# Optimization experiments

Hardware: AMD Instinct MI355X
Metric: run time of the kernel (lower is better)

The kernel has to match this reference:

```python
import jax, jax.numpy as jnp
import numpy as np

NEG_SLOPE = 0.2  # DGL GATConv default negative_slope


def gat_conv(x, W, attn_l, attn_r, bias, src, dst, n_nodes):
    """DGL-style GATConv. x:[N,F_in], W:[F_in,H*D], attn_l/attn_r/bias:[H,D].
    Returns [N,H,D]."""
    H, D = attn_l.shape
    feat = (x @ W).reshape(n_nodes, H, D)            # projected features
    el = jnp.sum(feat * attn_l, axis=-1)              # [N,H]
    er = jnp.sum(feat * attn_r, axis=-1)              # [N,H]
    e = jax.nn.leaky_relu(el[src] + er[dst], NEG_SLOPE)  # [E,H] per-edge score
    # edge softmax over incoming edges of each dst node (numerically stable)
    m = jax.ops.segment_max(e, dst, num_segments=n_nodes)   # [N,H]
    a = jnp.exp(e - m[dst])
    denom = jax.ops.segment_sum(a, dst, num_segments=n_nodes)
    alpha = a / denom[dst]                            # [E,H]
    msg = feat[src] * alpha[..., None]                # [E,H,D]
    out = jax.ops.segment_sum(msg, dst, num_segments=n_nodes)  # [N,H,D]
    return out + bias


def setup_inputs() -> dict:
    key = jax.random.key(0)
    ks = jax.random.split(key, 12)
    N, E = 50000, 800000
    F_in, D1, H1, F_out = 128, 32, 4, 64
    h = jax.random.normal(ks[0], (N, F_in), dtype=jnp.float32)
    src = jax.random.randint(ks[1], (E,), 0, N, dtype=jnp.int32)
    dst = jax.random.randint(ks[2], (E,), 0, N, dtype=jnp.int32)
    s1 = 1.0 / np.sqrt(F_in)
    s2 = 1.0 / np.sqrt(H1 * D1)
    W1 = jax.random.normal(ks[3], (F_in, H1 * D1), dtype=jnp.float32) * s1
    al1 = jax.random.normal(ks[4], (H1, D1), dtype=jnp.float32) * s1
    ar1 = jax.random.normal(ks[5], (H1, D1), dtype=jnp.float32) * s1
    b1 = jnp.zeros((H1, D1), dtype=jnp.float32)
    W2 = jax.random.normal(ks[6], (H1 * D1, 1 * F_out), dtype=jnp.float32) * s2
    al2 = jax.random.normal(ks[7], (1, F_out), dtype=jnp.float32) * s2
    ar2 = jax.random.normal(ks[8], (1, F_out), dtype=jnp.float32) * s2
    b2 = jnp.zeros((1, F_out), dtype=jnp.float32)
    return {"h": h, "src": src, "dst": dst,
            "W1": W1, "al1": al1, "ar1": ar1, "b1": b1,
            "W2": W2, "al2": al2, "ar2": ar2, "b2": b2}


def reference(h, src, dst, W1, al1, ar1, b1, W2, al2, ar2, b2):
    N = h.shape[0]
    x = gat_conv(h, W1, al1, ar1, b1, src, dst, N)   # [N,H,D]
    x = jax.nn.relu(x.reshape(N, -1))                # flatten heads + ReLU
    # dropout(p=0.2) is identity in eval mode
    x = gat_conv(x, W2, al2, ar2, b2, src, dst, N)   # [N,1,F_out]
    return x.squeeze(1)
```

## Files before the change

### kernel.cpp

```cpp
#include <hip/hip_runtime.h>

#define NEG_SLOPE 0.2f
#define CH 4096
#define DCAP 2048

__device__ inline unsigned short f2bf(float f) {
    unsigned u = __float_as_uint(f);
    unsigned r = (u + 0x7FFFu + ((u >> 16) & 1u)) >> 16;
    return (unsigned short)r;
}
__device__ inline unsigned pack2bf(float a, float b) {
    return (unsigned)f2bf(a) | ((unsigned)f2bf(b) << 16);
}
__device__ inline float bf2f(unsigned short s) {
    return __uint_as_float(((unsigned)s) << 16);
}
__device__ inline float bf2f_lo(unsigned u) { return __uint_as_float(u << 16); }
__device__ inline float bf2f_hi(unsigned u) { return __uint_as_float(u & 0xFFFF0000u); }
__device__ inline void wave_lds_fence() {
    asm volatile("s_waitcnt lgkmcnt(0)" ::: "memory");
}

__global__ __launch_bounds__(256) void bucketAB_kernel(const int* __restrict__ dst,
                                                       int* __restrict__ bucket_cnt,
                                                       int* __restrict__ bucket_base,
                                                       int* __restrict__ bucket_cursor,
                                                       int* __restrict__ row_start,
                                                       int N, int NB, int E) {
    __shared__ int lh[1024];
    __shared__ int psum[256];
    __shared__ int ticket_sh;
    const int tid = threadIdx.x;
    for (int i = tid; i < 1024; i += 256) lh[i] = 0;
    __syncthreads();
    const int base = blockIdx.x * CH;
    const int cnt = min(CH, E - base);
    for (int i = tid; i < cnt; i += 256) atomicAdd(&lh[dst[base + i] >> 6], 1);
    __syncthreads();
    for (int b = tid; b < NB; b += 256)
        if (lh[b]) atomicAdd(&bucket_cnt[b], lh[b]);
    __syncthreads();
    if (tid == 0) {
        __threadfence();
        ticket_sh = atomicAdd(&bucket_cnt[NB], 1);
    }
    __syncthreads();
    if (ticket_sh != (int)gridDim.x - 1) return;
    for (int i = tid; i < 1024; i += 256)
        lh[i] = (i < NB) ? atomicAdd(&bucket_cnt[i], 0) : 0;
    __syncthreads();
    int s0 = lh[tid * 4], s1 = lh[tid * 4 + 1], s2 = lh[tid * 4 + 2], s3 = lh[tid * 4 + 3];
    int tot = s0 + s1 + s2 + s3;
    psum[tid] = tot;
    __syncthreads();
    for (int off = 1; off < 256; off <<= 1) {
        int t = (tid >= off) ? psum[tid - off] : 0;
        __syncthreads();
        psum[tid] += t;
        __syncthreads();
    }
    int ebase = psum[tid] - tot;
    int e0 = ebase, e1 = ebase + s0, e2 = ebase + s0 + s1, e3 = ebase + s0 + s1 + s2;
    int i0 = tid * 4;
    if (i0 < NB)     { bucket_base[i0]     = e0; bucket_cursor[i0]     = e0; }
    if (i0 + 1 < NB) { bucket_base[i0 + 1] = e1; bucket_cursor[i0 + 1] = e1; }
    if (i0 + 2 < NB) { bucket_base[i0 + 2] = e2; bucket_cursor[i0 + 2] = e2; }
    if (i0 + 3 < NB) { bucket_base[i0 + 3] = e3; bucket_cursor[i0 + 3] = e3; }
    if (tid == 255) bucket_base[NB] = psum[255];
    if (tid == 0) row_start[N] = E;
}

__global__ __launch_bounds__(256) void csrC_gemm1_kernel(
    const int* __restrict__ src, const int* __restrict__ dst,
    int* __restrict__ bucket_cursor, unsigned* __restrict__ tmp, int E, int NB,
    int nchunks, const float* __restrict__ h, const float* __restrict__ W1,
    const float* __restrict__ al1, const float* __restrict__ ar1,
    unsigned short* __restrict__ feat1b, float* __restrict__ el1,
    float* __restrict__ er1, int N) {
    __shared__ __align__(16) int smem[8448];
    const int tid = threadIdx.x;
    if ((int)blockIdx.x < nchunks) {
        int* lh = smem;
        int* lex = smem + 1024;
        int* lcur = smem + 2048;
        int* gbase_sh = smem + 3072;
        int* psum = smem + 4096;
        unsigned* sortedv = (unsigned*)(smem + 4352);
        const int base_e = blockIdx.x * CH;
        const int cnt_e = min(CH, E - base_e);
        for (int i = tid; i < 1024; i += 256) lh[i] = 0;
        __syncthreads();
        for (int i = tid; i < cnt_e; i += 256) atomicAdd(&lh[dst[base_e + i] >> 6], 1);
        __syncthreads();
        int s0 = lh[tid * 4], s1 = lh[tid * 4 + 1], s2 = lh[tid * 4 + 2], s3 = lh[tid * 4 + 3];
        int tot = s0 + s1 + s2 + s3;
        psum[tid] = tot;
        __syncthreads();
        for (int off = 1; off < 256; off <<= 1) {
            int t = (tid >= off) ? psum[tid - off] : 0;
            __syncthreads();
            psum[tid] += t;
            __syncthreads();
        }
        int ebase = psum[tid] - tot;
        lex[tid * 4] = ebase;
        lex[tid * 4 + 1] = ebase + s0;
        lex[tid * 4 + 2] = ebase + s0 + s1;
        lex[tid * 4 + 3] = ebase + s0 + s1 + s2;
        __syncthreads();
        for (int b = tid; b < NB; b += 256) {
            int c = lh[b];
            gbase_sh[b] = c ? atomicAdd(&bucket_cursor[b], c) : 0;
            lcur[b] = 0;
        }
        __syncthreads();
        for (int i = tid; i < cnt_e; i += 256) {
            int e = base_e + i;
            int d = dst[e];
            unsigned b = (unsigned)d >> 6;
            int r = atomicAdd(&lcur[b], 1);
            sortedv[lex[b] + r] =
                (b << 22) | ((unsigned)(d & 63) << 16) | (unsigned)(src[e] & 0xFFFF);
        }
        __syncthreads();
        for (int i = tid; i < cnt_e; i += 256) {
            unsigned v = sortedv[i];
            int b = v >> 22;
            tmp[gbase_sh[b] + (i - lex[b])] = v;
        }
    } else {
        float* xs = (float*)smem;
        const int row0 = ((int)blockIdx.x - nchunks) * 64;
        {
            const float4* s4 = (const float4*)h;
            float4* d4 = (float4*)xs;
            int base4 = row0 * 32;
            int tot4 = N * 32;
            for (int i = tid; i < 2048; i += 256)
                if (base4 + i < tot4) d4[i] = s4[base4 + i];
        }
        __syncthreads();
        const int lane = tid & 31;
        const int c0 = lane * 4;
        const int r0 = (tid >> 5) * 8;
        float acc[8][4] = {};
#pragma unroll 4
        for (int k = 0; k < 128; ++k) {
            float4 w = *(const float4*)(W1 + k * 128 + c0);
#pragma unroll
            for (int r = 0; r < 8; ++r) {
                float x = xs[(r0 + r) * 128 + k];
                acc[r][0] = fmaf(x, w.x, acc[r][0]);
                acc[r][1] = fmaf(x, w.y, acc[r][1]);
                acc[r][2] = fmaf(x, w.z, acc[r][2]);
                acc[r][3] = fmaf(x, w.w, acc[r][3]);
            }
        }
        float4 alv = *(const float4*)(al1 + c0);
        float4 arv = *(const float4*)(ar1 + c0);
#pragma unroll
        for (int r = 0; r < 8; ++r) {
            int row = row0 + r0 + r;
            if (row < N) {
                ushort4 fb;
                fb.x = f2bf(acc[r][0]);
                fb.y = f2bf(acc[r][1]);
                fb.z = f2bf(acc[r][2]);
                fb.w = f2bf(acc[r][3]);
                *(ushort4*)(feat1b + (size_t)row * 128 + c0) = fb;
                float pl = acc[r][0] * alv.x + acc[r][1] * alv.y + acc[r][2] * alv.z +
                           acc[r][3] * alv.w;
                float pr = acc[r][0] * arv.x + acc[r][1] * arv.y + acc[r][2] * arv.z +
                           acc[r][3] * arv.w;
#pragma unroll
                for (int off = 4; off >= 1; off >>= 1) {
                    pl += __shfl_xor(pl, off, 32);
                    pr += __shfl_xor(pr, off, 32);
                }
                if ((lane & 7) == 0) {
                    el1[row * 4 + (lane >> 3)] = pl;
                    er1[row * 4 + (lane >> 3)] = pr;
                }
            }
        }
    }
}

__global__ __launch_bounds__(256) void bucketD_kernel(const unsigned* __restrict__ tmp,
                                                      const int* __restrict__ bucket_base,
                                                      int* __restrict__ srcs,
                                                      int* __restrict__ row_start,
                                                      int N, int NB) {
    __shared__ unsigned sval[DCAP];
    __shared__ int ssrc[DCAP];
    __shared__ int dh[64], dex[64], dcur[64];
    const int b = blockIdx.x;
    const int tid = threadIdx.x;
    const int gb = bucket_base[b], ge = bucket_base[b + 1];
    const int cnt = ge - gb;
    if (tid < 64) dh[tid] = 0;
    __syncthreads();
    if (cnt <= DCAP) {
        for (int i = tid; i < cnt; i += 256) {
            unsigned v = tmp[gb + i];
            sval[i] = v;
            atomicAdd(&dh[(v >> 16) & 63], 1);
        }
        __syncthreads();
        if (tid < 64) {
            int v = dh[tid], inc = v;
            for (int off = 1; off < 64; off <<= 1) {
                int t = __shfl_up(inc, off, 64);
                if (tid >= off) inc += t;
            }
            dex[tid] = inc - v;
            dcur[tid] = 0;
            int dglob = b * 64 + tid;
            if (dglob < N) row_start[dglob] = gb + inc - v;
        }
        __syncthreads();
        for (int i = tid; i < cnt; i += 256) {
            unsigned val = sval[i];
            int dl = (val >> 16) & 63;
            int r = atomicAdd(&dcur[dl], 1);
            ssrc[dex[dl] + r] = (int)(val & 0xFFFFu);
        }
        __syncthreads();
        for (int i = tid; i < cnt; i += 256) srcs[gb + i] = ssrc[i];
    } else {
        for (int i = tid; i < cnt; i += 256) atomicAdd(&dh[(tmp[gb + i] >> 16) & 63], 1);
        __syncthreads();
        if (tid < 64) {
            int v = dh[tid], inc = v;
            for (int off = 1; off < 64; off <<= 1) {
                int t = __shfl_up(inc, off, 64);
                if (tid >= off) inc += t;
            }
            dex[tid] = inc - v;
            dcur[tid] = 0;
            int dglob = b * 64 + tid;
            if (dglob < N) row_start[dglob] = gb + inc - v;
        }
        __syncthreads();
        for (int i = tid; i < cnt; i += 256) {
            unsigned val = tmp[gb + i];
            int dl = (val >> 16) & 63;
            int r = atomicAdd(&dcur[dl], 1);
            srcs[gb + dex[dl] + r] = (int)(val & 0xFFFFu);
        }
    }
}

__global__ __launch_bounds__(256) void gemm2_fused(const unsigned short* __restrict__ out1b,
                                                   const float* __restrict__ W2,
                                                   const float* __restrict__ al2,
                                                   const float* __restrict__ ar2,
                                                   unsigned short* __restrict__ feat2b,
                                                   float* __restrict__ el2,
                                                   float* __restrict__ er2, int N) {
    __shared__ float xs[64 * 128];
    const int tid = threadIdx.x;
    const int row0 = blockIdx.x * 64;
    {
        const uint4* s8 = (const uint4*)out1b;
        int base8 = row0 * 16;
        int tot8 = N * 16;
        for (int i = tid; i < 1024; i += 256)
            if (base8 + i < tot8) {
                uint4 v = s8[base8 + i];
                float* o = xs + i * 8;
                o[0] = bf2f_lo(v.x);
                o[1] = bf2f_hi(v.x);
                o[2] = bf2f_lo(v.y);
                o[3] = bf2f_hi(v.y);
                o[4] = bf2f_lo(v.z);
                o[5] = bf2f_hi(v.z);
                o[6] = bf2f_lo(v.w);
                o[7] = bf2f_hi(v.w);
            }
    }
    __syncthreads();
    const int lane = tid & 15;
    const int c0 = lane * 4;
    const int r0 = (tid >> 4) * 4;
    float acc[4][4] = {};
#pragma unroll 4
    for (int k = 0; k < 128; ++k) {
        float4 w = *(const float4*)(W2 + k * 64 + c0);
#pragma unroll
        for (int r = 0; r < 4; ++r) {
            float x = xs[(r0 + r) * 128 + k];
            acc[r][0] = fmaf(x, w.x, acc[r][0]);
            acc[r][1] = fmaf(x, w.y, acc[r][1]);
            acc[r][2] = fmaf(x, w.z, acc[r][2]);
            acc[r][3] = fmaf(x, w.w, acc[r][3]);
        }
    }
    float4 alv = *(const float4*)(al2 + c0);
    float4 arv = *(const float4*)(ar2 + c0);
#pragma unroll
    for (int r = 0; r < 4; ++r) {
        int row = row0 + r0 + r;
        if (row < N) {
            ushort4 fb;
            fb.x = f2bf(acc[r][0]);
            fb.y = f2bf(acc[r][1]);
            fb.z = f2bf(acc[r][2]);
            fb.w = f2bf(acc[r][3]);
            *(ushort4*)(feat2b + (size_t)row * 64 + c0) = fb;
            float pl = acc[r][0] * alv.x + acc[r][1] * alv.y + acc[r][2] * alv.z +
                       acc[r][3] * alv.w;
            float pr = acc[r][0] * arv.x + acc[r][1] * arv.y + acc[r][2] * arv.z +
                       acc[r][3] * arv.w;
#pragma unroll
            for (int off = 8; off >= 1; off >>= 1) {
                pl += __shfl_xor(pl, off, 16);
                pr += __shfl_xor(pr, off, 16);
            }
            if (lane == 0) {
                el2[row] = pl;
                er2[row] = pr;
            }
        }
    }
}

__global__ __launch_bounds__(256) void gather1_kernel(const int* __restrict__ row_start,
                                                      const int* __restrict__ srcs,
                                                      const float* __restrict__ el1,
                                                      const float* __restrict__ er1,
                                                      const unsigned short* __restrict__ feat1b,
                                                      const float* __restrict__ b1,
                                                      unsigned short* __restrict__ out1b,
                                                      int N) {
    __shared__ int s_sh[4][64];
    __shared__ float a_sh[4][256];
    const int tid = threadIdx.x;
    const int w = tid >> 6;
    const int lane = tid & 63;
    const int d = blockIdx.x * 4 + w;
    if (d >= N) return;
    const int beg = row_start[d], end = row_start[d + 1];
    const int q = lane >> 4;
    const int l16 = lane & 15;
    const int c0 = l16 * 8;
    const int h = l16 >> 2;
    float4 er4 = *(const float4*)(er1 + (size_t)d * 4);
    float acc[8] = {}, bcc[8] = {};
    float den = 0.f;
    for (int k0 = beg; k0 < end; k0 += 64) {
        const int M = min(64, end - k0);
        if (lane < M) {
            int s = srcs[k0 + lane];
            s_sh[w][lane] = s;
            float4 el4 = *(const float4*)(el1 + (size_t)s * 4);
            float v0 = el4.x + er4.x;
            float v1 = el4.y + er4.y;
            float v2 = el4.z + er4.z;
            float v3 = el4.w + er4.w;
            v0 = v0 > 0.f ? v0 : NEG_SLOPE * v0;
            v1 = v1 > 0.f ? v1 : NEG_SLOPE * v1;
            v2 = v2 > 0.f ? v2 : NEG_SLOPE * v2;
            v3 = v3 > 0.f ? v3 : NEG_SLOPE * v3;
            a_sh[w][lane * 4 + 0] = __expf(v0);
            a_sh[w][lane * 4 + 1] = __expf(v1);
            a_sh[w][lane * 4 + 2] = __expf(v2);
            a_sh[w][lane * 4 + 3] = __expf(v3);
        }
        wave_lds_fence();
        int e = q;
        for (; e + 4 < M; e += 8) {
            int s0 = s_sh[w][e], s1 = s_sh[w][e + 4];
            float a0 = a_sh[w][e * 4 + h];
            float a1 = a_sh[w][(e + 4) * 4 + h];
            uint4 f0 = *(const uint4*)(feat1b + (size_t)s0 * 128 + c0);
            uint4 f1 = *(const uint4*)(feat1b + (size_t)s1 * 128 + c0);
            den += a0 + a1;
            acc[0] = fmaf(bf2f_lo(f0.x), a0, acc[0]);
            acc[1] = fmaf(bf2f_hi(f0.x), a0, acc[1]);
            acc[2] = fmaf(bf2f_lo(f0.y), a0, acc[2]);
            acc[3] = fmaf(bf2f_hi(f0.y), a0, acc[3]);
            acc[4] = fmaf(bf2f_lo(f0.z), a0, acc[4]);
            acc[5] = fmaf(bf2f_hi(f0.z), a0, acc[5]);
            acc[6] = fmaf(bf2f_lo(f0.w), a0, acc[6]);
            acc[7] = fmaf(bf2f_hi(f0.w), a0, acc[7]);
            bcc[0] = fmaf(bf2f_lo(f1.x), a1, bcc[0]);
            bcc[1] = fmaf(bf2f_hi(f1.x), a1, bcc[1]);
            bcc[2] = fmaf(bf2f_lo(f1.y), a1, bcc[2]);
            bcc[3] = fmaf(bf2f_hi(f1.y), a1, bcc[3]);
            bcc[4] = fmaf(bf2f_lo(f1.z), a1, bcc[4]);
            bcc[5] = fmaf(bf2f_hi(f1.z), a1, bcc[5]);
            bcc[6] = fmaf(bf2f_lo(f1.w), a1, bcc[6]);
            bcc[7] = fmaf(bf2f_hi(f1.w), a1, bcc[7]);
        }
        while (e < M) {
            int s0 = s_sh[w][e];
            float a0 = a_sh[w][e * 4 + h];
            uint4 f0 = *(const uint4*)(feat1b + (size_t)s0 * 128 + c0);
            den += a0;
            acc[0] = fmaf(bf2f_lo(f0.x), a0, acc[0]);
            acc[1] = fmaf(bf2f_hi(f0.x), a0, acc[1]);
            acc[2] = fmaf(bf2f_lo(f0.y), a0, acc[2]);
            acc[3] = fmaf(bf2f_hi(f0.y), a0, acc[3]);
            acc[4] = fmaf(bf2f_lo(f0.z), a0, acc[4]);
            acc[5] = fmaf(bf2f_hi(f0.z), a0, acc[5]);
            acc[6] = fmaf(bf2f_lo(f0.w), a0, acc[6]);
            acc[7] = fmaf(bf2f_hi(f0.w), a0, acc[7]);
            e += 4;
        }
        wave_lds_fence();
    }
#pragma unroll
    for (int j = 0; j < 8; ++j) {
        acc[j] += bcc[j];
        acc[j] += __shfl_xor(acc[j], 16, 64);
        acc[j] += __shfl_xor(acc[j], 32, 64);
    }
    den += __shfl_xor(den, 16, 64);
    den += __shfl_xor(den, 32, 64);
    if (q == 0) {
        float inv = (end > beg) ? 1.f / den : 0.f;
        float4 bv0 = *(const float4*)(b1 + c0);
        float4 bv1 = *(const float4*)(b1 + c0 + 4);
        uint4 o;
        o.x = pack2bf(fmaxf(acc[0] * inv + bv0.x, 0.f), fmaxf(acc[1] * inv + bv0.y, 0.f));
        o.y = pack2bf(fmaxf(acc[2] * inv + bv0.z, 0.f), fmaxf(acc[3] * inv + bv0.w, 0.f));
        o.z = pack2bf(fmaxf(acc[4] * inv + bv1.x, 0.f), fmaxf(acc[5] * inv + bv1.y, 0.f));
        o.w = pack2bf(fmaxf(acc[6] * inv + bv1.z, 0.f), fmaxf(acc[7] * inv + bv1.w, 0.f));
        *(uint4*)(out1b + (size_t)d * 128 + c0) = o;
    }
}

__global__ __launch_bounds__(256) void gather2_kernel(const int* __restrict__ row_start,
                                                      const int* __restrict__ srcs,
                                                      const float* __restrict__ el2,
                                                      const float* __restrict__ er2,
                                                      const unsigned short* __restrict__ feat2b,
                                                      const float* __restrict__ b2,
                                                      float* __restrict__ out2, int N) {
    __shared__ int s_sh[4][64];
    __shared__ float a_sh[4][64];
    const int tid = threadIdx.x;
    const int w = tid >> 6;
    const int lane = tid & 63;
    const int d = blockIdx.x * 4 + w;
    if (d >= N) return;
    const int beg = row_start[d], end = row_start[d + 1];
    const int q = lane >> 4;
    const int l16 = lane & 15;
    const int c0 = l16 * 4;
    const float er_d = er2[d];
    float acc[4] = {}, bcc[4] = {};
    float den = 0.f;
    for (int k0 = beg; k0 < end; k0 += 64) {
        const int M = min(64, end - k0);
        if (lane < M) {
            int s = srcs[k0 + lane];
            s_sh[w][lane] = s;
            float v = el2[s] + er_d;
            v = v > 0.f ? v : NEG_SLOPE * v;
            a_sh[w][lane] = __expf(v);
        }
        wave_lds_fence();
        int e = q;
        for (; e + 4 < M; e += 8) {
            int s0 = s_sh[w][e], s1 = s_sh[w][e + 4];
            float a0 = a_sh[w][e], a1 = a_sh[w][e + 4];
            uint2 f0 = *(const uint2*)(feat2b + (size_t)s0 * 64 + c0);
            uint2 f1 = *(const uint2*)(feat2b + (size_t)s1 * 64 + c0);
            den += a0 + a1;
            acc[0] = fmaf(bf2f_lo(f0.x), a0, acc[0]);
            acc[1] = fmaf(bf2f_hi(f0.x), a0, acc[1]);
            acc[2] = fmaf(bf2f_lo(f0.y), a0, acc[2]);
            acc[3] = fmaf(bf2f_hi(f0.y), a0, acc[3]);
            bcc[0] = fmaf(bf2f_lo(f1.x), a1, bcc[0]);
            bcc[1] = fmaf(bf2f_hi(f1.x), a1, bcc[1]);
            bcc[2] = fmaf(bf2f_lo(f1.y), a1, bcc[2]);
            bcc[3] = fmaf(bf2f_hi(f1.y), a1, bcc[3]);
        }
        while (e < M) {
            int s0 = s_sh[w][e];
            float a0 = a_sh[w][e];
            uint2 f0 = *(const uint2*)(feat2b + (size_t)s0 * 64 + c0);
            den += a0;
            acc[0] = fmaf(bf2f_lo(f0.x), a0, acc[0]);
            acc[1] = fmaf(bf2f_hi(f0.x), a0, acc[1]);
            acc[2] = fmaf(bf2f_lo(f0.y), a0, acc[2]);
            acc[3] = fmaf(bf2f_hi(f0.y), a0, acc[3]);
            e += 4;
        }
        wave_lds_fence();
    }
#pragma unroll
    for (int j = 0; j < 4; ++j) {
        acc[j] += bcc[j];
        acc[j] += __shfl_xor(acc[j], 16, 64);
        acc[j] += __shfl_xor(acc[j], 32, 64);
    }
    den += __shfl_xor(den, 16, 64);
    den += __shfl_xor(den, 32, 64);
    if (q == 0) {
        float inv = (end > beg) ? 1.f / den : 0.f;
        float4 bv = *(const float4*)(b2 + c0);
        *(float4*)(out2 + (size_t)d * 64 + c0) =
            make_float4(acc[0] * inv + bv.x, acc[1] * inv + bv.y, acc[2] * inv + bv.z,
                        acc[3] * inv + bv.w);
    }
}

extern "C" void kernel_launch(void* const* d_in, const int* in_sizes, int n_in,
                              void* d_out, int out_size, void* d_ws, size_t ws_size,
                              hipStream_t stream) {
    const float* h   = (const float*)d_in[0];
    const int*   src = (const int*)d_in[1];
    const int*   dst = (const int*)d_in[2];
    const float* W1  = (const float*)d_in[3];
    const float* al1 = (const float*)d_in[4];
    const float* ar1 = (const float*)d_in[5];
    const float* b1  = (const float*)d_in[6];
    const float* W2  = (const float*)d_in[7];
    const float* al2 = (const float*)d_in[8];
    const float* ar2 = (const float*)d_in[9];
    const float* b2  = (const float*)d_in[10];

    const int N = in_sizes[0] / 128;
    const int E = in_sizes[1];
    const int NB = (N + 63) >> 6;

    char* ws = (char*)d_ws;
    size_t off = 0;
    auto alloc = [&](size_t elems) -> void* {
        void* p = (void*)(ws + off);
        off += ((elems * 4 + 255) / 256) * 256;
        return p;
    };
    int* bucket_cnt    = (int*)alloc(NB + 1);
    int* bucket_base   = (int*)alloc(NB + 1);
    int* bucket_cursor = (int*)alloc(NB);
    unsigned* tmp      = (unsigned*)alloc(E);
    int* srcs          = (int*)alloc(E);
    int* row_start     = (int*)alloc(N + 1);
    float* el1   = (float*)alloc((size_t)N * 4);
    float* er1   = (float*)alloc((size_t)N * 4);
    unsigned short* feat1b = (unsigned short*)alloc((size_t)N * 64);
    unsigned short* out1b  = (unsigned short*)alloc((size_t)N * 64);
    float* el2   = (float*)alloc(N);
    float* er2   = (float*)alloc(N);
    unsigned short* feat2b = (unsigned short*)alloc((size_t)N * 32);
    float* out2  = (float*)d_out;

    const int nchunks = (E + CH - 1) / CH;
    const int gemm1_blocks = (N + 63) / 64;

    hipMemsetAsync(bucket_cnt, 0, (size_t)(NB + 1) * 4, stream);
    bucketAB_kernel<<<nchunks, 256, 0, stream>>>(dst, bucket_cnt, bucket_base,
                                                 bucket_cursor, row_start, N, NB, E);
    csrC_gemm1_kernel<<<nchunks + gemm1_blocks, 256, 0, stream>>>(
        src, dst, bucket_cursor, tmp, E, NB, nchunks, h, W1, al1, ar1, feat1b, el1,
        er1, N);
    bucketD_kernel<<<NB, 256, 0, stream>>>(tmp, bucket_base, srcs, row_start, N, NB);

    gather1_kernel<<<(N + 3) / 4, 256, 0, stream>>>(row_start, srcs, el1, er1, feat1b,
                                                    b1, out1b, N);

    gemm2_fused<<<(N + 63) / 64, 256, 0, stream>>>(out1b, W2, al2, ar2, feat2b, el2,
                                                   er2, N);
    gather2_kernel<<<(N + 3) / 4, 256, 0, stream>>>(row_start, srcs, el2, er2, feat2b,
                                                    b2, out2, N);
}
```

Before: 221.2 us.

## Fuse bucket histogram into CSR scatter kernel with grid-wide spin barrier; widen gather2 loads

The separate bucket counting/prefix kernel is merged into the CSR-scatter+GEMM1 kernel. Each chunk block publishes its histogram, the last block to arrive computes the bucket prefix sums and sets a ready flag, and all chunk blocks spin on that flag before claiming scatter offsets. This removes one kernel launch and one re-read of dst, but it depends on every chunk block being co-resident, which risks deadlock if they are not. Separately, gather2 now has each lane load 8 bf16 features (uint4) instead of 4, with one extra shuffle stage, so fewer, wider loads are issued per edge.

```diff
diff --git a/kernel.cpp b/kernel.cpp
--- a/kernel.cpp
+++ b/kernel.cpp
@@ -21,59 +21,12 @@
     asm volatile("s_waitcnt lgkmcnt(0)" ::: "memory");
 }
 
-__global__ __launch_bounds__(256) void bucketAB_kernel(const int* __restrict__ dst,
-                                                       int* __restrict__ bucket_cnt,
-                                                       int* __restrict__ bucket_base,
-                                                       int* __restrict__ bucket_cursor,
-                                                       int* __restrict__ row_start,
-                                                       int N, int NB, int E) {
-    __shared__ int lh[1024];
-    __shared__ int psum[256];
-    __shared__ int ticket_sh;
-    const int tid = threadIdx.x;
-    for (int i = tid; i < 1024; i += 256) lh[i] = 0;
-    __syncthreads();
-    const int base = blockIdx.x * CH;
-    const int cnt = min(CH, E - base);
-    for (int i = tid; i < cnt; i += 256) atomicAdd(&lh[dst[base + i] >> 6], 1);
-    __syncthreads();
-    for (int b = tid; b < NB; b += 256)
-        if (lh[b]) atomicAdd(&bucket_cnt[b], lh[b]);
-    __syncthreads();
-    if (tid == 0) {
-        __threadfence();
-        ticket_sh = atomicAdd(&bucket_cnt[NB], 1);
-    }
-    __syncthreads();
-    if (ticket_sh != (int)gridDim.x - 1) return;
-    for (int i = tid; i < 1024; i += 256)
-        lh[i] = (i < NB) ? atomicAdd(&bucket_cnt[i], 0) : 0;
-    __syncthreads();
-    int s0 = lh[tid * 4], s1 = lh[tid * 4 + 1], s2 = lh[tid * 4 + 2], s3 = lh[tid * 4 + 3];
-    int tot = s0 + s1 + s2 + s3;
-    psum[tid] = tot;
-    __syncthreads();
-    for (int off = 1; off < 256; off <<= 1) {
-        int t = (tid >= off) ? psum[tid - off] : 0;
-        __syncthreads();
-        psum[tid] += t;
-        __syncthreads();
-    }
-    int ebase = psum[tid] - tot;
-    int e0 = ebase, e1 = ebase + s0, e2 = ebase + s0 + s1, e3 = ebase + s0 + s1 + s2;
-    int i0 = tid * 4;
-    if (i0 < NB)     { bucket_base[i0]     = e0; bucket_cursor[i0]     = e0; }
-    if (i0 + 1 < NB) { bucket_base[i0 + 1] = e1; bucket_cursor[i0 + 1] = e1; }
-    if (i0 + 2 < NB) { bucket_base[i0 + 2] = e2; bucket_cursor[i0 + 2] = e2; }
-    if (i0 + 3 < NB) { bucket_base[i0 + 3] = e3; bucket_cursor[i0 + 3] = e3; }
-    if (tid == 255) bucket_base[NB] = psum[255];
-    if (tid == 0) row_start[N] = E;
-}
-
-__global__ __launch_bounds__(256) void csrC_gemm1_kernel(
+__global__ __launch_bounds__(256) void csrABC_gemm1_kernel(
     const int* __restrict__ src, const int* __restrict__ dst,
-    int* __restrict__ bucket_cursor, unsigned* __restrict__ tmp, int E, int NB,
-    int nchunks, const float* __restrict__ h, const float* __restrict__ W1,
+    int* __restrict__ bucket_cnt, int* __restrict__ bucket_base,
+    int* __restrict__ bucket_cursor, int* __restrict__ row_start,
+    unsigned* __restrict__ tmp, int E, int NB, int nchunks,
+    const float* __restrict__ h, const float* __restrict__ W1,
     const float* __restrict__ al1, const float* __restrict__ ar1,
     unsigned short* __restrict__ feat1b, float* __restrict__ el1,
     float* __restrict__ er1, int N) {
@@ -92,6 +45,45 @@
         __syncthreads();
         for (int i = tid; i < cnt_e; i += 256) atomicAdd(&lh[dst[base_e + i] >> 6], 1);
         __syncthreads();
+        for (int b = tid; b < NB; b += 256)
+            if (lh[b]) atomicAdd(&bucket_cnt[b], lh[b]);
+        __syncthreads();
+        __shared__ int ticket_sh;
+        if (tid == 0) {
+            __threadfence();
+            ticket_sh = atomicAdd(&bucket_cnt[NB], 1);
+        }
+        __syncthreads();
+        if (ticket_sh == nchunks - 1) {
+            for (int i = tid; i < 1024; i += 256)
+                lcur[i] = (i < NB) ? atomicAdd(&bucket_cnt[i], 0) : 0;
+            __syncthreads();
+            int c0s = lcur[tid * 4], c1s = lcur[tid * 4 + 1], c2s = lcur[tid * 4 + 2],
+                c3s = lcur[tid * 4 + 3];
+            int tot = c0s + c1s + c2s + c3s;
+            psum[tid] = tot;
+            __syncthreads();
+            for (int off = 1; off < 256; off <<= 1) {
+                int t = (tid >= off) ? psum[tid - off] : 0;
+                __syncthreads();
+                psum[tid] += t;
+                __syncthreads();
+            }
+            int eb = psum[tid] - tot;
+            int i0 = tid * 4;
+            if (i0 < NB)     { bucket_base[i0]     = eb;               atomicExch(&bucket_cursor[i0], eb); }
+            if (i0 + 1 < NB) { bucket_base[i0 + 1] = eb + c0s;         atomicExch(&bucket_cursor[i0 + 1], eb + c0s); }
+            if (i0 + 2 < NB) { bucket_base[i0 + 2] = eb + c0s + c1s;   atomicExch(&bucket_cursor[i0 + 2], eb + c0s + c1s); }
+            if (i0 + 3 < NB) { bucket_base[i0 + 3] = eb + c0s + c1s + c2s;
+                               atomicExch(&bucket_cursor[i0 + 3], eb + c0s + c1s + c2s); }
+            if (tid == 255) bucket_base[NB] = psum[255];
+            if (tid == 0) row_start[N] = E;
+            __syncthreads();
+            if (tid == 0) {
+                __threadfence();
+                atomicExch(&bucket_cnt[NB + 1], 1);
+            }
+        }
         int s0 = lh[tid * 4], s1 = lh[tid * 4 + 1], s2 = lh[tid * 4 + 2], s3 = lh[tid * 4 + 3];
         int tot = s0 + s1 + s2 + s3;
         psum[tid] = tot;
@@ -108,17 +100,24 @@
         lex[tid * 4 + 2] = ebase + s0 + s1;
         lex[tid * 4 + 3] = ebase + s0 + s1 + s2;
         __syncthreads();
+        __shared__ int ready_sh;
+        if (tid == 0) {
+            while (atomicAdd(&bucket_cnt[NB + 1], 0) == 0) {}
+            ready_sh = 1;
+        }
+        __syncthreads();
+        (void)ready_sh;
         for (int b = tid; b < NB; b += 256) {
             int c = lh[b];
             gbase_sh[b] = c ? atomicAdd(&bucket_cursor[b], c) : 0;
-            lcur[b] = 0;
+            lh[b] = 0;
         }
         __syncthreads();
         for (int i = tid; i < cnt_e; i += 256) {
             int e = base_e + i;
             int d = dst[e];
             unsigned b = (unsigned)d >> 6;
-            int r = atomicAdd(&lcur[b], 1);
+            int r = atomicAdd(&lh[b], 1);
             sortedv[lex[b] + r] =
                 (b << 22) | ((unsigned)(d & 63) << 16) | (unsigned)(src[e] & 0xFFFF);
         }
@@ -446,11 +445,11 @@
     const int d = blockIdx.x * 4 + w;
     if (d >= N) return;
     const int beg = row_start[d], end = row_start[d + 1];
-    const int q = lane >> 4;
-    const int l16 = lane & 15;
-    const int c0 = l16 * 4;
+    const int oct = lane >> 3;
+    const int l8 = lane & 7;
+    const int c0 = l8 * 8;
     const float er_d = er2[d];
-    float acc[4] = {}, bcc[4] = {};
+    float acc[8] = {}, bcc[8] = {};
     float den = 0.f;
     for (int k0 = beg; k0 < end; k0 += 64) {
         const int M = min(64, end - k0);
@@ -462,49 +461,67 @@
             a_sh[w][lane] = __expf(v);
         }
         wave_lds_fence();
-        int e = q;
-        for (; e + 4 < M; e += 8) {
-            int s0 = s_sh[w][e], s1 = s_sh[w][e + 4];
-            float a0 = a_sh[w][e], a1 = a_sh[w][e + 4];
-            uint2 f0 = *(const uint2*)(feat2b + (size_t)s0 * 64 + c0);
-            uint2 f1 = *(const uint2*)(feat2b + (size_t)s1 * 64 + c0);
+        int e = oct;
+        for (; e + 8 < M; e += 16) {
+            int s0 = s_sh[w][e], s1 = s_sh[w][e + 8];
+            float a0 = a_sh[w][e], a1 = a_sh[w][e + 8];
+            uint4 f0 = *(const uint4*)(feat2b + (size_t)s0 * 64 + c0);
+            uint4 f1 = *(const uint4*)(feat2b + (size_t)s1 * 64 + c0);
             den += a0 + a1;
             acc[0] = fmaf(bf2f_lo(f0.x), a0, acc[0]);
             acc[1] = fmaf(bf2f_hi(f0.x), a0, acc[1]);
             acc[2] = fmaf(bf2f_lo(f0.y), a0, acc[2]);
             acc[3] = fmaf(bf2f_hi(f0.y), a0, acc[3]);
+            acc[4] = fmaf(bf2f_lo(f0.z), a0, acc[4]);
+            acc[5] = fmaf(bf2f_hi(f0.z), a0, acc[5]);
+            acc[6] = fmaf(bf2f_lo(f0.w), a0, acc[6]);
+            acc[7] = fmaf(bf2f_hi(f0.w), a0, acc[7]);
             bcc[0] = fmaf(bf2f_lo(f1.x), a1, bcc[0]);
             bcc[1] = fmaf(bf2f_hi(f1.x), a1, bcc[1]);
             bcc[2] = fmaf(bf2f_lo(f1.y), a1, bcc[2]);
             bcc[3] = fmaf(bf2f_hi(f1.y), a1, bcc[3]);
+            bcc[4] = fmaf(bf2f_lo(f1.z), a1, bcc[4]);
+            bcc[5] = fmaf(bf2f_hi(f1.z), a1, bcc[5]);
+            bcc[6] = fmaf(bf2f_lo(f1.w), a1, bcc[6]);
+            bcc[7] = fmaf(bf2f_hi(f1.w), a1, bcc[7]);
         }
         while (e < M) {
             int s0 = s_sh[w][e];
             float a0 = a_sh[w][e];
-            uint2 f0 = *(const uint2*)(feat2b + (size_t)s0 * 64 + c0);
+            uint4 f0 = *(const uint4*)(feat2b + (size_t)s0 * 64 + c0);
             den += a0;
             acc[0] = fmaf(bf2f_lo(f0.x), a0, acc[0]);
             acc[1] = fmaf(bf2f_hi(f0.x), a0, acc[1]);
             acc[2] = fmaf(bf2f_lo(f0.y), a0, acc[2]);
             acc[3] = fmaf(bf2f_hi(f0.y), a0, acc[3]);
-            e += 4;
+            acc[4] = fmaf(bf2f_lo(f0.z), a0, acc[4]);
+            acc[5] = fmaf(bf2f_hi(f0.z), a0, acc[5]);
+            acc[6] = fmaf(bf2f_lo(f0.w), a0, acc[6]);
+            acc[7] = fmaf(bf2f_hi(f0.w), a0, acc[7]);
+            e += 8;
         }
         wave_lds_fence();
     }
 #pragma unroll
-    for (int j = 0; j < 4; ++j) {
+    for (int j = 0; j < 8; ++j) {
         acc[j] += bcc[j];
+        acc[j] += __shfl_xor(acc[j], 8, 64);
         acc[j] += __shfl_xor(acc[j], 16, 64);
         acc[j] += __shfl_xor(acc[j], 32, 64);
     }
+    den += __shfl_xor(den, 8, 64);
     den += __shfl_xor(den, 16, 64);
     den += __shfl_xor(den, 32, 64);
-    if (q == 0) {
+    if (oct == 0) {
         float inv = (end > beg) ? 1.f / den : 0.f;
-        float4 bv = *(const float4*)(b2 + c0);
+        float4 bv0 = *(const float4*)(b2 + c0);
+        float4 bv1 = *(const float4*)(b2 + c0 + 4);
         *(float4*)(out2 + (size_t)d * 64 + c0) =
-            make_float4(acc[0] * inv + bv.x, acc[1] * inv + bv.y, acc[2] * inv + bv.z,
-                        acc[3] * inv + bv.w);
+            make_float4(acc[0] * inv + bv0.x, acc[1] * inv + bv0.y,
+                        acc[2] * inv + bv0.z, acc[3] * inv + bv0.w);
+        *(float4*)(out2 + (size_t)d * 64 + c0 + 4) =
+            make_float4(acc[4] * inv + bv1.x, acc[5] * inv + bv1.y,
+                        acc[6] * inv + bv1.z, acc[7] * inv + bv1.w);
     }
 }
 
@@ -534,7 +551,7 @@
         off += ((elems * 4 + 255) / 256) * 256;
         return p;
     };
-    int* bucket_cnt    = (int*)alloc(NB + 1);
+    int* bucket_cnt    = (int*)alloc(NB + 2);
     int* bucket_base   = (int*)alloc(NB + 1);
     int* bucket_cursor = (int*)alloc(NB);
     unsigned* tmp      = (unsigned*)alloc(E);
@@ -552,12 +569,10 @@
     const int nchunks = (E + CH - 1) / CH;
     const int gemm1_blocks = (N + 63) / 64;
 
-    hipMemsetAsync(bucket_cnt, 0, (size_t)(NB + 1) * 4, stream);
-    bucketAB_kernel<<<nchunks, 256, 0, stream>>>(dst, bucket_cnt, bucket_base,
-                                                 bucket_cursor, row_start, N, NB, E);
-    csrC_gemm1_kernel<<<nchunks + gemm1_blocks, 256, 0, stream>>>(
-        src, dst, bucket_cursor, tmp, E, NB, nchunks, h, W1, al1, ar1, feat1b, el1,
-        er1, N);
+    hipMemsetAsync(bucket_cnt, 0, (size_t)(NB + 2) * 4, stream);
+    csrABC_gemm1_kernel<<<nchunks + gemm1_blocks, 256, 0, stream>>>(
+        src, dst, bucket_cnt, bucket_base, bucket_cursor, row_start, tmp, E, NB,
+        nchunks, h, W1, al1, ar1, feat1b, el1, er1, N);
     bucketD_kernel<<<NB, 256, 0, stream>>>(tmp, bucket_base, srcs, row_start, N, NB);
 
     gather1_kernel<<<(N + 3) / 4, 256, 0, stream>>>(row_start, srcs, el1, er1, feat1b,
```

Result: faster. 210.5 us (median of 2 runs) (-4.9%).
